# Performance work log

Hardware: AMD Instinct MI355X
Metric: run time of the kernel (lower is better)

## Reference

```python
import jax, jax.numpy as jnp
import numpy as np

B, DIN, DOUT, E, H, K = 8192, 1024, 1024, 8, 128, 2

def setup_inputs() -> dict:
    key = jax.random.key(0)
    ks = jax.random.split(key, 6)
    s = 0.02
    return {
        "x": jax.random.normal(ks[0], (B, DIN), jnp.float32),
        "w1": jax.random.normal(ks[1], (DIN, H), jnp.float32) * s,
        "b1": jnp.zeros((H,), jnp.float32),
        "wg": jax.random.normal(ks[2], (DIN, H), jnp.float32) * s,
        "bg": jnp.zeros((H,), jnp.float32),
        "w2": jax.random.normal(ks[3], (H, E), jnp.float32) * s,
        "b2": jnp.zeros((E,), jnp.float32),
        "we": jax.random.normal(ks[4], (E, DIN, DOUT), jnp.float32) * s,
        "be": jnp.zeros((E, DOUT), jnp.float32),
    }

def reference(x, w1, b1, wg, bg, w2, b2, we, be):
    Bx = x.shape[0]
    Eo = we.shape[0]
    Do = we.shape[2]
    # Router with GLU; NOTE: softmax over BATCH dim (dim=0), as in source.
    h = (x @ w1 + b1) * jax.nn.relu(x @ wg + bg)
    h = jax.nn.relu(h)
    l = jax.nn.softmax(x=(h @ w2 + b2), axis=0)  # [B, E]
    batch_K = -(-K * Bx) // Eo  # ceil(K/E * B), static
    # top-k tokens per expert (along batch dim)
    ws_t, ib_t = jax.lax.top_k(l.T, batch_K)  # [E, bK]
    ws, ib = ws_t.T, ib_t.T                   # [bK, E]
    nws = jax.nn.softmax(ws, axis=0)          # renorm over selected tokens
    # dispatch: gather selected tokens for all experts at once
    sel = x[ib]                                # [bK, E, DIN]
    eo = jnp.einsum('ked,edo->keo', sel, we) + be  # [bK, E, DOUT]
    eo = eo * nws[:, :, None]
    # combine (concat_sum): per-expert scatter-set + shared scatter-add sum
    e_idx = jnp.broadcast_to(jnp.arange(Eo)[None, :], ib.shape)  # [bK, E]
    out_e = jnp.zeros((Eo, Bx, Do), x.dtype).at[e_idx, ib].set(eo)
    temp_sum = jnp.zeros((Bx, Do), x.dtype).at[ib].add(eo)
    out_e = out_e + temp_sum[None]
    return out_e.transpose(1, 0, 2).reshape(Bx, Eo * Do)
```

## Files before the change

kernel.cpp:

```cpp
#include <hip/hip_runtime.h>
#include <math.h>

#define B_TOK 8192
#define D_IN 1024
#define D_OUT 1024
#define N_E 8
#define N_H 128
#define SEL 2048

using bf16x8 = __attribute__((ext_vector_type(8))) short;
using floatx4 = __attribute__((ext_vector_type(4))) float;

__device__ __forceinline__ unsigned short f2bf(float f) {
  unsigned u = __float_as_uint(f);
  u = (u + 0x7FFFu + ((u >> 16) & 1u)) >> 16;
  return (unsigned short)u;
}

__device__ __forceinline__ void async_cp16(const void* g, void* l) {
  __builtin_amdgcn_global_load_lds((__attribute__((address_space(1))) void*)g,
                                   (__attribute__((address_space(3))) void*)l,
                                   16, 0, 0);
}

__global__ __launch_bounds__(256) void k_cast_x(const float* __restrict__ x,
                                                unsigned short* __restrict__ xb) {
  int i = (blockIdx.x * 256 + threadIdx.x) * 8;
  float4 a = *(const float4*)(x + i);
  float4 b = *(const float4*)(x + i + 4);
  ushort4 lo; lo.x = f2bf(a.x); lo.y = f2bf(a.y); lo.z = f2bf(a.z); lo.w = f2bf(a.w);
  ushort4 hi; hi.x = f2bf(b.x); hi.y = f2bf(b.y); hi.z = f2bf(b.z); hi.w = f2bf(b.w);
  *(ushort4*)(xb + i) = lo;
  *(ushort4*)(xb + i + 4) = hi;
}

__global__ __launch_bounds__(256) void k_cast_weT(const float* __restrict__ we,
                                                  unsigned short* __restrict__ web) {
  __shared__ float tile[64][68];
  const int e = blockIdx.z;
  const float* wsrc = we + (size_t)e * D_IN * D_OUT;
  unsigned short* wdst = web + (size_t)e * D_OUT * D_IN;
  const int t = threadIdx.x;
  const int r = t >> 4;
  const int c = (t & 15) * 4;
  const int d0 = blockIdx.x * 64, o0 = blockIdx.y * 64;
#pragma unroll
  for (int p = 0; p < 4; ++p) {
    float4 v = *(const float4*)(wsrc + (size_t)(d0 + r + 16 * p) * D_OUT + o0 + c);
    tile[r + 16 * p][c] = v.x; tile[r + 16 * p][c + 1] = v.y;
    tile[r + 16 * p][c + 2] = v.z; tile[r + 16 * p][c + 3] = v.w;
  }
  __syncthreads();
#pragma unroll
  for (int p = 0; p < 4; ++p) {
    int orow = r + 16 * p;
    ushort4 v;
    v.x = f2bf(tile[c + 0][orow]); v.y = f2bf(tile[c + 1][orow]);
    v.z = f2bf(tile[c + 2][orow]); v.w = f2bf(tile[c + 3][orow]);
    *(ushort4*)(wdst + (size_t)(o0 + orow) * D_IN + d0 + c) = v;
  }
}

__global__ __launch_bounds__(256) void k_router_h(const float* __restrict__ x,
                                                  const float* __restrict__ w1,
                                                  const float* __restrict__ b1,
                                                  const float* __restrict__ wg,
                                                  const float* __restrict__ bg,
                                                  float* __restrict__ h) {
  __shared__ float xs[32][36];
  __shared__ float ws1[32][128];
  __shared__ float wsg[32][128];
  const int t = threadIdx.x;
  const int b0 = blockIdx.x * 32;
  const int tg = t >> 5;
  const int og = t & 31;
  double d1[4][4] = {}; double dg[4][4] = {};
  for (int k0 = 0; k0 < D_IN; k0 += 32) {
    __syncthreads();
    {
      int r = t >> 3, c = (t & 7) * 4;
      float4 v = *(const float4*)(x + (size_t)(b0 + r) * D_IN + k0 + c);
      *(float4*)(&xs[r][c]) = v;
    }
    {
      int r = t >> 5, c = (t & 31) * 4;
#pragma unroll
      for (int p = 0; p < 4; ++p) {
        *(float4*)(&ws1[r + 8 * p][c]) = *(const float4*)(w1 + (size_t)(k0 + r + 8 * p) * N_H + c);
        *(float4*)(&wsg[r + 8 * p][c]) = *(const float4*)(wg + (size_t)(k0 + r + 8 * p) * N_H + c);
      }
    }
    __syncthreads();
    float a1[4][4] = {}; float ag[4][4] = {};
    for (int k = 0; k < 32; k += 4) {
      float xk[4][4];
#pragma unroll
      for (int i = 0; i < 4; ++i) {
        float4 v = *(const float4*)(&xs[tg * 4 + i][k]);
        xk[i][0] = v.x; xk[i][1] = v.y; xk[i][2] = v.z; xk[i][3] = v.w;
      }
#pragma unroll
      for (int kk = 0; kk < 4; ++kk) {
        float4 w1v = *(const float4*)(&ws1[k + kk][og * 4]);
        float4 wgv = *(const float4*)(&wsg[k + kk][og * 4]);
        float wa1[4] = {w1v.x, w1v.y, w1v.z, w1v.w};
        float wag[4] = {wgv.x, wgv.y, wgv.z, wgv.w};
#pragma unroll
        for (int i = 0; i < 4; ++i) {
#pragma unroll
          for (int j = 0; j < 4; ++j) {
            a1[i][j] += xk[i][kk] * wa1[j];
            ag[i][j] += xk[i][kk] * wag[j];
          }
        }
      }
    }
#pragma unroll
    for (int i = 0; i < 4; ++i)
#pragma unroll
      for (int j = 0; j < 4; ++j) { d1[i][j] += a1[i][j]; dg[i][j] += ag[i][j]; }
  }
  float4 b1v = *(const float4*)(b1 + og * 4);
  float4 bgv = *(const float4*)(bg + og * 4);
  float b1a[4] = {b1v.x, b1v.y, b1v.z, b1v.w};
  float bga[4] = {bgv.x, bgv.y, bgv.z, bgv.w};
#pragma unroll
  for (int i = 0; i < 4; ++i) {
    float hv[4];
#pragma unroll
    for (int j = 0; j < 4; ++j) {
      float a = (float)d1[i][j] + b1a[j];
      float g = (float)dg[i][j] + bga[j];
      g = fmaxf(g, 0.f);
      hv[j] = fmaxf(a * g, 0.f);
    }
    *(float4*)(h + (size_t)(b0 + tg * 4 + i) * N_H + og * 4) = *(float4*)hv;
  }
}

__global__ __launch_bounds__(256) void k_logits(const float* __restrict__ h,
                                                const float* __restrict__ w2,
                                                const float* __restrict__ b2,
                                                double* __restrict__ logits) {
  __shared__ float w2s[N_H * N_E];
  const int t = threadIdx.x;
  ((float4*)w2s)[t] = ((const float4*)w2)[t];
  __syncthreads();
  const int token = blockIdx.x * 64 + (t >> 2);
  const int part = t & 3;
  double acc[8] = {};
  const float* hrow = h + (size_t)token * N_H + part * 32;
#pragma unroll
  for (int k = 0; k < 32; k += 4) {
    float4 hv = *(const float4*)(hrow + k);
    float ha[4] = {hv.x, hv.y, hv.z, hv.w};
#pragma unroll
    for (int l = 0; l < 4; ++l) {
      int kk = part * 32 + k + l;
#pragma unroll
      for (int e2 = 0; e2 < 8; ++e2)
        acc[e2] += (double)ha[l] * (double)w2s[kk * N_E + e2];
    }
  }
#pragma unroll
  for (int e2 = 0; e2 < 8; ++e2) {
    acc[e2] += __shfl_down(acc[e2], 1);
    acc[e2] += __shfl_down(acc[e2], 2);
  }
  if (part == 0) {
#pragma unroll
    for (int e2 = 0; e2 < 8; ++e2)
      logits[(size_t)token * N_E + e2] = acc[e2] + (double)b2[e2];
  }
}

__global__ __launch_bounds__(256) void k_topk(const double* __restrict__ logits,
                                              int* __restrict__ ib, float* __restrict__ nws,
                                              int* __restrict__ slot) {
  const int e = blockIdx.x;
  const int t = threadIdx.x;
  __shared__ double redd[4];
  __shared__ int redi[4];
  __shared__ unsigned redu[4];
  __shared__ int s_cnt;

  double lv[32];
#pragma unroll
  for (int i = 0; i < 32; ++i) lv[i] = logits[(size_t)(t + i * 256) * N_E + e];

  double m = -1e300;
#pragma unroll
  for (int i = 0; i < 32; ++i) m = fmax(m, lv[i]);
  for (int o = 32; o; o >>= 1) m = fmax(m, __shfl_down(m, o));
  __syncthreads();
  if ((t & 63) == 0) redd[t >> 6] = m;
  __syncthreads();
  const double maxl = fmax(fmax(redd[0], redd[1]), fmax(redd[2], redd[3]));

  double s = 0.0;
#pragma unroll
  for (int i = 0; i < 32; ++i) s += exp(lv[i] - maxl);
  for (int o = 32; o; o >>= 1) s += __shfl_down(s, o);
  __syncthreads();
  if ((t & 63) == 0) redd[t >> 6] = s;
  __syncthreads();
  const double sum = redd[0] + redd[1] + redd[2] + redd[3];

  unsigned kr[32];
#pragma unroll
  for (int i = 0; i < 32; ++i) {
    float lf = (float)(exp(lv[i] - maxl) / sum);
    kr[i] = __float_as_uint(lf);
  }

  unsigned thr = 0;
  for (int bit = 31; bit >= 0; --bit) {
    unsigned trial = thr | (1u << bit);
    int c = 0;
#pragma unroll
    for (int i = 0; i < 32; ++i) c += (kr[i] >= trial) ? 1 : 0;
    for (int o = 32; o; o >>= 1) c += __shfl_down(c, o);
    __syncthreads();
    if ((t & 63) == 0) redi[t >> 6] = c;
    __syncthreads();
    c = redi[0] + redi[1] + redi[2] + redi[3];
    if (c >= SEL) thr = trial;
  }

  int c1 = 0;
#pragma unroll
  for (int i = 0; i < 32; ++i) c1 += (kr[i] > thr) ? 1 : 0;
  for (int o = 32; o; o >>= 1) c1 += __shfl_down(c1, o);
  __syncthreads();
  if ((t & 63) == 0) redi[t >> 6] = c1;
  __syncthreads();
  c1 = redi[0] + redi[1] + redi[2] + redi[3];
  const int need = SEL - c1;

  int cut = 0;
  for (int bit = 12; bit >= 0; --bit) {
    int trial = cut | (1 << bit);
    int c = 0;
#pragma unroll
    for (int i = 0; i < 32; ++i) c += (kr[i] == thr && (t + i * 256) < trial) ? 1 : 0;
    for (int o = 32; o; o >>= 1) c += __shfl_down(c, o);
    __syncthreads();
    if ((t & 63) == 0) redi[t >> 6] = c;
    __syncthreads();
    c = redi[0] + redi[1] + redi[2] + redi[3];
    if (c < need) cut = trial;
  }

  unsigned mk = 0;
#pragma unroll
  for (int i = 0; i < 32; ++i) mk = (kr[i] > mk) ? kr[i] : mk;
  for (int o = 32; o; o >>= 1) { unsigned v = __shfl_down(mk, o); mk = (v > mk) ? v : mk; }
  __syncthreads();
  if ((t & 63) == 0) redu[t >> 6] = mk;
  __syncthreads();
  mk = redu[0]; if (redu[1] > mk) mk = redu[1]; if (redu[2] > mk) mk = redu[2]; if (redu[3] > mk) mk = redu[3];
  const double maxw = (double)__uint_as_float(mk);

  double ss = 0.0;
#pragma unroll
  for (int i = 0; i < 32; ++i) {
    int idx = t + i * 256;
    bool sel = (kr[i] > thr) || (kr[i] == thr && idx <= cut);
    if (sel) ss += exp((double)__uint_as_float(kr[i]) - maxw);
  }
  for (int o = 32; o; o >>= 1) ss += __shfl_down(ss, o);
  __syncthreads();
  if ((t & 63) == 0) redd[t >> 6] = ss;
  __syncthreads();
  const double ssum = redd[0] + redd[1] + redd[2] + redd[3];

  if (t == 0) s_cnt = 0;
#pragma unroll
  for (int i = 0; i < 32; ++i) slot[(size_t)(t + i * 256) * N_E + e] = -1;
  __syncthreads();
  for (int i = 0; i < 32; ++i) {
    int idx = t + i * 256;
    bool sel = (kr[i] > thr) || (kr[i] == thr && idx <= cut);
    if (sel) {
      int pos = atomicAdd(&s_cnt, 1);
      ib[e * SEL + pos] = idx;
      nws[e * SEL + pos] = (float)(exp((double)__uint_as_float(kr[i]) - maxw) / ssum);
      slot[(size_t)idx * N_E + e] = pos;
    }
  }
}

__global__ __launch_bounds__(256) void k_expert_gemm(const unsigned short* __restrict__ xb,
                                                     const unsigned short* __restrict__ web,
                                                     const float* __restrict__ be,
                                                     const int* __restrict__ ib,
                                                     const float* __restrict__ nws,
                                                     float* __restrict__ eo) {
  __shared__ unsigned short As[128 * 64];
  __shared__ unsigned short Bs[128 * 64];
  __shared__ int rowidx[128];
  __shared__ float nwss[128];
  const int e = blockIdx.z;
  const int bm = blockIdx.x * 128;
  const int bn = blockIdx.y * 128;
  const int t = threadIdx.x;
  const int wave = t >> 6, lane = t & 63;
  if (t < 128) {
    rowidx[t] = ib[e * SEL + bm + t];
    nwss[t] = nws[e * SEL + bm + t];
  }
  __syncthreads();
  const unsigned short* wbase = web + (size_t)e * D_IN * D_OUT;
  const int chunk = lane & 7;
  const unsigned short* aptr[4];
  const unsigned short* bptr[4];
  unsigned short* adst[4];
  unsigned short* bdst[4];
#pragma unroll
  for (int c = 0; c < 4; ++c) {
    int row = c * 32 + wave * 8 + (lane >> 3);
    aptr[c] = xb + (size_t)rowidx[row] * D_IN + chunk * 8;
    bptr[c] = wbase + (size_t)(bn + row) * D_IN + chunk * 8;
    adst[c] = As + row * 64 + chunk * 8;
    bdst[c] = Bs + row * 64 + chunk * 8;
  }
  floatx4 acc[4][4] = {};
  const int wm = wave >> 1, wn = wave & 1;
  const int fr = lane & 15, fq = lane >> 4;

  for (int k0 = 0; k0 < D_IN; k0 += 64) {
#pragma unroll
    for (int c = 0; c < 4; ++c) {
      async_cp16(aptr[c] + k0, adst[c]);
      async_cp16(bptr[c] + k0, bdst[c]);
    }
    __syncthreads();
#pragma unroll
    for (int kk = 0; kk < 2; ++kk) {
      bf16x8 af[4], bfr[4];
#pragma unroll
      for (int mt = 0; mt < 4; ++mt)
        af[mt] = *(const bf16x8*)(As + (wm * 64 + mt * 16 + fr) * 64 + kk * 32 + fq * 8);
#pragma unroll
      for (int nt = 0; nt < 4; ++nt)
        bfr[nt] = *(const bf16x8*)(Bs + (wn * 64 + nt * 16 + fr) * 64 + kk * 32 + fq * 8);
#pragma unroll
      for (int mt = 0; mt < 4; ++mt)
#pragma unroll
        for (int nt = 0; nt < 4; ++nt)
          acc[mt][nt] = __builtin_amdgcn_mfma_f32_16x16x32_bf16(af[mt], bfr[nt], acc[mt][nt], 0, 0, 0);
    }
    __syncthreads();
  }
  float bev[4];
#pragma unroll
  for (int nt = 0; nt < 4; ++nt) bev[nt] = be[e * D_OUT + bn + wn * 64 + nt * 16 + fr];
#pragma unroll
  for (int mt = 0; mt < 4; ++mt) {
#pragma unroll
    for (int r = 0; r < 4; ++r) {
      int lrow = wm * 64 + mt * 16 + fq * 4 + r;
      float nw = nwss[lrow];
      size_t rbase = ((size_t)e * SEL + bm + lrow) * D_OUT;
#pragma unroll
      for (int nt = 0; nt < 4; ++nt) {
        int cc = bn + wn * 64 + nt * 16 + fr;
        eo[rbase + cc] = (acc[mt][nt][r] + bev[nt]) * nw;
      }
    }
  }
}

__global__ __launch_bounds__(256) void k_combine(const float* __restrict__ eo,
                                                 const int* __restrict__ slot,
                                                 float* __restrict__ out) {
  const int b = blockIdx.x;
  const int t = threadIdx.x;
  __shared__ int ss[8];
  if (t < 8) ss[t] = slot[(size_t)b * N_E + t];
  __syncthreads();
  const int d0 = t * 4;
  float vx[8], vy[8], vz[8], vw[8];
  float tx = 0.f, ty = 0.f, tz = 0.f, tw = 0.f;
#pragma unroll
  for (int e = 0; e < 8; ++e) {
    int k = ss[e];
    if (k >= 0) {
      float4 v = *(const float4*)(eo + ((size_t)e * SEL + k) * D_OUT + d0);
      vx[e] = v.x; vy[e] = v.y; vz[e] = v.z; vw[e] = v.w;
      tx += v.x; ty += v.y; tz += v.z; tw += v.w;
    } else {
      vx[e] = 0.f; vy[e] = 0.f; vz[e] = 0.f; vw[e] = 0.f;
    }
  }
#pragma unroll
  for (int e = 0; e < 8; ++e) {
    float4 o;
    o.x = tx + vx[e]; o.y = ty + vy[e]; o.z = tz + vz[e]; o.w = tw + vw[e];
    *(float4*)(out + (size_t)b * (N_E * D_OUT) + e * D_OUT + d0) = o;
  }
}

extern "C" void kernel_launch(void* const* d_in, const int* in_sizes, int n_in,
                              void* d_out, int out_size, void* d_ws, size_t ws_size,
                              hipStream_t stream) {
  const float* x  = (const float*)d_in[0];
  const float* w1 = (const float*)d_in[1];
  const float* b1 = (const float*)d_in[2];
  const float* wg = (const float*)d_in[3];
  const float* bg = (const float*)d_in[4];
  const float* w2 = (const float*)d_in[5];
  const float* b2 = (const float*)d_in[6];
  const float* we = (const float*)d_in[7];
  const float* be = (const float*)d_in[8];
  float* out = (float*)d_out;

  char* ws = (char*)d_ws;
  size_t off = 0;
  auto alloc = [&](size_t bytes) -> void* {
    void* p = ws + off;
    off += (bytes + 255) & ~(size_t)255;
    return p;
  };
  unsigned short* xb  = (unsigned short*)alloc((size_t)B_TOK * D_IN * 2);
  unsigned short* web = (unsigned short*)alloc((size_t)N_E * D_IN * D_OUT * 2);
  float* eo     = (float*)alloc((size_t)N_E * SEL * D_OUT * 4);
  float* h      = (float*)alloc((size_t)B_TOK * N_H * 4);
  double* lgts  = (double*)alloc((size_t)B_TOK * N_E * 8);
  int* ibuf     = (int*)alloc((size_t)N_E * SEL * 4);
  float* nws    = (float*)alloc((size_t)N_E * SEL * 4);
  int* slot     = (int*)alloc((size_t)B_TOK * N_E * 4);
  if (off > ws_size) return;

  hipLaunchKernelGGL(k_cast_x, dim3(B_TOK * D_IN / (256 * 8)), dim3(256), 0, stream, x, xb);
  hipLaunchKernelGGL(k_cast_weT, dim3(16, 16, N_E), dim3(256), 0, stream, we, web);
  hipLaunchKernelGGL(k_router_h, dim3(B_TOK / 32), dim3(256), 0, stream, x, w1, b1, wg, bg, h);
  hipLaunchKernelGGL(k_logits, dim3(B_TOK / 64), dim3(256), 0, stream, h, w2, b2, lgts);
  hipLaunchKernelGGL(k_topk, dim3(N_E), dim3(256), 0, stream, lgts, ibuf, nws, slot);
  hipLaunchKernelGGL(k_expert_gemm, dim3(SEL / 128, D_OUT / 128, N_E), dim3(256), 0, stream,
                     xb, web, be, ibuf, nws, eo);
  hipLaunchKernelGGL(k_combine, dim3(B_TOK), dim3(256), 0, stream, eo, slot, out);
}
```

Before: 555.4 us.

## Fuse x cast and logits into router kernel, store expert outputs as bf16

Removes the separate x-to-bf16 cast kernel and the logits kernel by folding both into the router GEMM. The router now handles 16 tokens per block, casting x tiles as it loads them and reducing the h@w2 projection with wave shuffles, so the h buffer never goes to global memory. Expert outputs are stored as bf16 instead of fp32, which halves the write and gather traffic in the combine step. The cost is reduced output precision and smaller router tiles, which give less weight reuse per block.

```diff
diff --git a/kernel.cpp b/kernel.cpp
--- a/kernel.cpp
+++ b/kernel.cpp
@@ -17,21 +17,14 @@
   return (unsigned short)u;
 }
 
+__device__ __forceinline__ float bf2f(unsigned short h) {
+  return __uint_as_float(((unsigned)h) << 16);
+}
+
 __device__ __forceinline__ void async_cp16(const void* g, void* l) {
   __builtin_amdgcn_global_load_lds((__attribute__((address_space(1))) void*)g,
                                    (__attribute__((address_space(3))) void*)l,
                                    16, 0, 0);
-}
-
-__global__ __launch_bounds__(256) void k_cast_x(const float* __restrict__ x,
-                                                unsigned short* __restrict__ xb) {
-  int i = (blockIdx.x * 256 + threadIdx.x) * 8;
-  float4 a = *(const float4*)(x + i);
-  float4 b = *(const float4*)(x + i + 4);
-  ushort4 lo; lo.x = f2bf(a.x); lo.y = f2bf(a.y); lo.z = f2bf(a.z); lo.w = f2bf(a.w);
-  ushort4 hi; hi.x = f2bf(b.x); hi.y = f2bf(b.y); hi.z = f2bf(b.z); hi.w = f2bf(b.w);
-  *(ushort4*)(xb + i) = lo;
-  *(ushort4*)(xb + i + 4) = hi;
 }
 
 __global__ __launch_bounds__(256) void k_cast_weT(const float* __restrict__ we,
@@ -61,26 +54,35 @@
   }
 }
 
-__global__ __launch_bounds__(256) void k_router_h(const float* __restrict__ x,
-                                                  const float* __restrict__ w1,
-                                                  const float* __restrict__ b1,
-                                                  const float* __restrict__ wg,
-                                                  const float* __restrict__ bg,
-                                                  float* __restrict__ h) {
-  __shared__ float xs[32][36];
+__global__ __launch_bounds__(256) void k_router(const float* __restrict__ x,
+                                                const float* __restrict__ w1,
+                                                const float* __restrict__ b1,
+                                                const float* __restrict__ wg,
+                                                const float* __restrict__ bg,
+                                                const float* __restrict__ w2,
+                                                const float* __restrict__ b2,
+                                                unsigned short* __restrict__ xb,
+                                                double* __restrict__ logits) {
+  __shared__ float xs[16][36];
   __shared__ float ws1[32][128];
   __shared__ float wsg[32][128];
+  __shared__ float w2s[N_H * N_E];
   const int t = threadIdx.x;
-  const int b0 = blockIdx.x * 32;
+  const int b0 = blockIdx.x * 16;
   const int tg = t >> 5;
   const int og = t & 31;
-  double d1[4][4] = {}; double dg[4][4] = {};
+
+  ((float4*)w2s)[t] = ((const float4*)w2)[t];
+
+  double d1[2][4] = {}; double dg[2][4] = {};
   for (int k0 = 0; k0 < D_IN; k0 += 32) {
     __syncthreads();
-    {
+    if (t < 128) {
       int r = t >> 3, c = (t & 7) * 4;
       float4 v = *(const float4*)(x + (size_t)(b0 + r) * D_IN + k0 + c);
       *(float4*)(&xs[r][c]) = v;
+      ushort4 u; u.x = f2bf(v.x); u.y = f2bf(v.y); u.z = f2bf(v.z); u.w = f2bf(v.w);
+      *(ushort4*)(xb + (size_t)(b0 + r) * D_IN + k0 + c) = u;
     }
     {
       int r = t >> 5, c = (t & 31) * 4;
@@ -91,12 +93,12 @@
       }
     }
     __syncthreads();
-    float a1[4][4] = {}; float ag[4][4] = {};
+    float a1[2][4] = {}; float ag[2][4] = {};
     for (int k = 0; k < 32; k += 4) {
-      float xk[4][4];
-#pragma unroll
-      for (int i = 0; i < 4; ++i) {
-        float4 v = *(const float4*)(&xs[tg * 4 + i][k]);
+      float xk[2][4];
+#pragma unroll
+      for (int i = 0; i < 2; ++i) {
+        float4 v = *(const float4*)(&xs[tg * 2 + i][k]);
         xk[i][0] = v.x; xk[i][1] = v.y; xk[i][2] = v.z; xk[i][3] = v.w;
       }
 #pragma unroll
@@ -106,7 +108,7 @@
         float wa1[4] = {w1v.x, w1v.y, w1v.z, w1v.w};
         float wag[4] = {wgv.x, wgv.y, wgv.z, wgv.w};
 #pragma unroll
-        for (int i = 0; i < 4; ++i) {
+        for (int i = 0; i < 2; ++i) {
 #pragma unroll
           for (int j = 0; j < 4; ++j) {
             a1[i][j] += xk[i][kk] * wa1[j];
@@ -116,61 +118,53 @@
       }
     }
 #pragma unroll
-    for (int i = 0; i < 4; ++i)
+    for (int i = 0; i < 2; ++i)
 #pragma unroll
       for (int j = 0; j < 4; ++j) { d1[i][j] += a1[i][j]; dg[i][j] += ag[i][j]; }
   }
+
   float4 b1v = *(const float4*)(b1 + og * 4);
   float4 bgv = *(const float4*)(bg + og * 4);
   float b1a[4] = {b1v.x, b1v.y, b1v.z, b1v.w};
   float bga[4] = {bgv.x, bgv.y, bgv.z, bgv.w};
-#pragma unroll
-  for (int i = 0; i < 4; ++i) {
-    float hv[4];
+  float hv[2][4];
+#pragma unroll
+  for (int i = 0; i < 2; ++i) {
 #pragma unroll
     for (int j = 0; j < 4; ++j) {
       float a = (float)d1[i][j] + b1a[j];
       float g = (float)dg[i][j] + bga[j];
       g = fmaxf(g, 0.f);
-      hv[j] = fmaxf(a * g, 0.f);
-    }
-    *(float4*)(h + (size_t)(b0 + tg * 4 + i) * N_H + og * 4) = *(float4*)hv;
-  }
-}
-
-__global__ __launch_bounds__(256) void k_logits(const float* __restrict__ h,
-                                                const float* __restrict__ w2,
-                                                const float* __restrict__ b2,
-                                                double* __restrict__ logits) {
-  __shared__ float w2s[N_H * N_E];
-  const int t = threadIdx.x;
-  ((float4*)w2s)[t] = ((const float4*)w2)[t];
-  __syncthreads();
-  const int token = blockIdx.x * 64 + (t >> 2);
-  const int part = t & 3;
-  double acc[8] = {};
-  const float* hrow = h + (size_t)token * N_H + part * 32;
-#pragma unroll
-  for (int k = 0; k < 32; k += 4) {
-    float4 hv = *(const float4*)(hrow + k);
-    float ha[4] = {hv.x, hv.y, hv.z, hv.w};
-#pragma unroll
-    for (int l = 0; l < 4; ++l) {
-      int kk = part * 32 + k + l;
-#pragma unroll
-      for (int e2 = 0; e2 < 8; ++e2)
-        acc[e2] += (double)ha[l] * (double)w2s[kk * N_E + e2];
-    }
-  }
-#pragma unroll
-  for (int e2 = 0; e2 < 8; ++e2) {
-    acc[e2] += __shfl_down(acc[e2], 1);
-    acc[e2] += __shfl_down(acc[e2], 2);
-  }
-  if (part == 0) {
-#pragma unroll
-    for (int e2 = 0; e2 < 8; ++e2)
-      logits[(size_t)token * N_E + e2] = acc[e2] + (double)b2[e2];
+      hv[i][j] = fmaxf(a * g, 0.f);
+    }
+  }
+
+  double lp[2][8] = {};
+#pragma unroll
+  for (int i = 0; i < 2; ++i) {
+#pragma unroll
+    for (int j = 0; j < 4; ++j) {
+      double hj = (double)hv[i][j];
+      int kk = og * 4 + j;
+#pragma unroll
+      for (int e = 0; e < 8; ++e)
+        lp[i][e] += hj * (double)w2s[kk * N_E + e];
+    }
+  }
+#pragma unroll
+  for (int o = 16; o; o >>= 1) {
+#pragma unroll
+    for (int i = 0; i < 2; ++i)
+#pragma unroll
+      for (int e = 0; e < 8; ++e)
+        lp[i][e] += __shfl_down(lp[i][e], o);
+  }
+  if (og == 0) {
+#pragma unroll
+    for (int i = 0; i < 2; ++i)
+#pragma unroll
+      for (int e = 0; e < 8; ++e)
+        logits[(size_t)(b0 + tg * 2 + i) * N_E + e] = lp[i][e] + (double)b2[e];
   }
 }
 
@@ -295,7 +289,7 @@
                                                      const float* __restrict__ be,
                                                      const int* __restrict__ ib,
                                                      const float* __restrict__ nws,
-                                                     float* __restrict__ eo) {
+                                                     unsigned short* __restrict__ eo) {
   __shared__ unsigned short As[128 * 64];
   __shared__ unsigned short Bs[128 * 64];
   __shared__ int rowidx[128];
@@ -365,13 +359,13 @@
 #pragma unroll
       for (int nt = 0; nt < 4; ++nt) {
         int cc = bn + wn * 64 + nt * 16 + fr;
-        eo[rbase + cc] = (acc[mt][nt][r] + bev[nt]) * nw;
+        eo[rbase + cc] = f2bf((acc[mt][nt][r] + bev[nt]) * nw);
       }
     }
   }
 }
 
-__global__ __launch_bounds__(256) void k_combine(const float* __restrict__ eo,
+__global__ __launch_bounds__(256) void k_combine(const unsigned short* __restrict__ eo,
                                                  const int* __restrict__ slot,
                                                  float* __restrict__ out) {
   const int b = blockIdx.x;
@@ -386,9 +380,9 @@
   for (int e = 0; e < 8; ++e) {
     int k = ss[e];
     if (k >= 0) {
-      float4 v = *(const float4*)(eo + ((size_t)e * SEL + k) * D_OUT + d0);
-      vx[e] = v.x; vy[e] = v.y; vz[e] = v.z; vw[e] = v.w;
-      tx += v.x; ty += v.y; tz += v.z; tw += v.w;
+      ushort4 u = *(const ushort4*)(eo + ((size_t)e * SEL + k) * D_OUT + d0);
+      vx[e] = bf2f(u.x); vy[e] = bf2f(u.y); vz[e] = bf2f(u.z); vw[e] = bf2f(u.w);
+      tx += vx[e]; ty += vy[e]; tz += vz[e]; tw += vw[e];
     } else {
       vx[e] = 0.f; vy[e] = 0.f; vz[e] = 0.f; vw[e] = 0.f;
     }
@@ -424,18 +418,16 @@
   };
   unsigned short* xb  = (unsigned short*)alloc((size_t)B_TOK * D_IN * 2);
   unsigned short* web = (unsigned short*)alloc((size_t)N_E * D_IN * D_OUT * 2);
-  float* eo     = (float*)alloc((size_t)N_E * SEL * D_OUT * 4);
-  float* h      = (float*)alloc((size_t)B_TOK * N_H * 4);
+  unsigned short* eo  = (unsigned short*)alloc((size_t)N_E * SEL * D_OUT * 2);
   double* lgts  = (double*)alloc((size_t)B_TOK * N_E * 8);
   int* ibuf     = (int*)alloc((size_t)N_E * SEL * 4);
   float* nws    = (float*)alloc((size_t)N_E * SEL * 4);
   int* slot     = (int*)alloc((size_t)B_TOK * N_E * 4);
   if (off > ws_size) return;
 
-  hipLaunchKernelGGL(k_cast_x, dim3(B_TOK * D_IN / (256 * 8)), dim3(256), 0, stream, x, xb);
   hipLaunchKernelGGL(k_cast_weT, dim3(16, 16, N_E), dim3(256), 0, stream, we, web);
-  hipLaunchKernelGGL(k_router_h, dim3(B_TOK / 32), dim3(256), 0, stream, x, w1, b1, wg, bg, h);
-  hipLaunchKernelGGL(k_logits, dim3(B_TOK / 64), dim3(256), 0, stream, h, w2, b2, lgts);
+  hipLaunchKernelGGL(k_router, dim3(B_TOK / 16), dim3(256), 0, stream,
+                     x, w1, b1, wg, bg, w2, b2, xb, lgts);
   hipLaunchKernelGGL(k_topk, dim3(N_E), dim3(256), 0, stream, lgts, ibuf, nws, slot);
   hipLaunchKernelGGL(k_expert_gemm, dim3(SEL / 128, D_OUT / 128, N_E), dim3(256), 0, stream,
                      xb, web, be, ibuf, nws, eo);
```

Measured after the change: 535.2 us. 3.6% less time.
